# Performance work log

Measured on AMD Instinct MI355X. Metric: run time of the kernel, lower is better.

## Reference

```python
import jax, jax.numpy as jnp
import numpy as np

NUM_EMBEDDINGS = 1024
EMBEDDING_DIM = 64


def setup_inputs() -> dict:
    key = jax.random.key(0)
    kx, kw = jax.random.split(key)
    x = jax.random.normal(kx, (16, 4096, EMBEDDING_DIM), dtype=jnp.float32)
    # torch init: uniform(-1/K, 1/K)
    bound = 1.0 / NUM_EMBEDDINGS
    weight = jax.random.uniform(kw, (NUM_EMBEDDINGS, EMBEDDING_DIM),
                                dtype=jnp.float32, minval=-bound, maxval=bound)
    return {"x": x, "weight": weight}


def reference(x, weight):
    flat_x = x.reshape(-1, EMBEDDING_DIM)                      # [N, D]
    x_sq = jnp.sum(flat_x ** 2, axis=1, keepdims=True)
    w_sq = jnp.sum(weight ** 2, axis=1)[None, :]
    distances = x_sq - 2.0 * (flat_x @ weight.T) + w_sq
    encoding_indices = jnp.argmin(distances, axis=1)           # [N]
    quantized = weight[encoding_indices]                       # [N, D]
    e_latent_loss = jnp.mean((jax.lax.stop_gradient(quantized) - flat_x) ** 2)
    q_latent_loss = jnp.mean((quantized - jax.lax.stop_gradient(flat_x)) ** 2)
    loss = q_latent_loss + 0.25 * e_latent_loss
    # straight-through estimator
    quantized = flat_x + jax.lax.stop_gradient(quantized - flat_x)
    return quantized.reshape(x.shape), encoding_indices, loss
```

## Files before the change

### kernel.cpp

```cpp
#include <hip/hip_runtime.h>
#include <math.h>

#define EMB_D 64
#define MARGIN 6.0e-5f
#define SBIAS 0.5f

typedef float  f32x4  __attribute__((ext_vector_type(4)));
typedef short  bf16x8 __attribute__((ext_vector_type(8)));

__device__ __forceinline__ unsigned short f2bf(float f) {
    unsigned int u = __float_as_uint(f);
    return (unsigned short)((u + 0x7FFFu + ((u >> 16) & 1u)) >> 16);
}
__device__ __forceinline__ float bf2f(unsigned short h) {
    return __uint_as_float(((unsigned int)h) << 16);
}

union Pack8 { ushort u[8]; bf16x8 v; uint4 q; };

__device__ __forceinline__ bf16x8 ldbf8(const unsigned short* p) {
    union { uint4 u; bf16x8 v; } c;
    c.u = *(const uint4*)p;
    return c.v;
}

__global__ __launch_bounds__(256)
void vq_prepw_kernel(const float* __restrict__ w,
                     unsigned short* __restrict__ wt_hi,
                     unsigned short* __restrict__ wt_lo,
                     float* __restrict__ wsq, float* __restrict__ loss_out,
                     int K) {
    const int i = blockIdx.x * 256 + threadIdx.x;
    if (i == 0) loss_out[0] = 0.f;
    if (i >= K * 8) return;
    const int krow = i >> 3, q = i & 7;
    const int dest = ((krow >> 6) << 9) + (((krow >> 4) & 3) << 7) + (q << 4)
                   + (krow & 15);
    const float* src = w + (size_t)krow * EMB_D + q * 8;
    Pack8 h, l;
#pragma unroll
    for (int j = 0; j < 8; ++j) {
        const float f = src[j];
        h.u[j] = f2bf(f);
        l.u[j] = f2bf(f - bf2f(h.u[j]));
    }
    ((uint4*)wt_hi)[dest] = h.q;
    ((uint4*)wt_lo)[dest] = l.q;

    if (i < K) {
        const float* wr = w + (size_t)i * EMB_D;
        float r[8];
#pragma unroll
        for (int j = 0; j < 8; ++j) r[j] = __fmul_rn(wr[j], wr[j]);
#pragma unroll
        for (int t = 1; t < 8; ++t)
#pragma unroll
            for (int j = 0; j < 8; ++j)
                r[j] = __fadd_rn(r[j], __fmul_rn(wr[t * 8 + j], wr[t * 8 + j]));
        float a = __fadd_rn(__fadd_rn(r[0], r[1]), __fadd_rn(r[2], r[3]));
        float b = __fadd_rn(__fadd_rn(r[4], r[5]), __fadd_rn(r[6], r[7]));
        wsq[i] = __fadd_rn(a, b);
    }
}

__global__ __launch_bounds__(256, 2)
void vq_fused_kernel(const float* __restrict__ x,
                     const unsigned short* __restrict__ wt_hi,
                     const unsigned short* __restrict__ wt_lo,
                     const float* __restrict__ wsq,
                     const float* __restrict__ w,
                     float* __restrict__ out, float* __restrict__ loss_out,
                     int K, int N, float scale) {
    const int tid  = threadIdx.x;
    const int lane = tid & 63;
    const int wave = tid >> 6;
    const int quad = lane >> 4;
    const int c16  = lane & 15;
    const int rowbase = blockIdx.x * 128 + wave * 32;

    __shared__ __align__(16) char arena[20480];
    uint4* sh4     = (uint4*)arena;
    uint4* sl4     = (uint4*)(arena + 8192);
    float* wsq_lds = (float*)(arena + 16384);
    typedef unsigned MpArr[32][19];
    MpArr* Mp1 = (MpArr*)arena;
    MpArr* Mp2 = (MpArr*)(arena + 9728);

    __shared__ int kf[128], strow[128], k2row[128];

    Pack8 AH0[2], AL0[2], AH1[2], AL1[2];
#pragma unroll
    for (int t = 0; t < 2; ++t) {
        const float* xrow =
            x + (size_t)(rowbase + t * 16 + c16) * EMB_D + quad * 8;
#pragma unroll
        for (int j = 0; j < 8; ++j) {
            const float f0 = xrow[j];
            AH0[t].u[j] = f2bf(f0);
            AL0[t].u[j] = f2bf(f0 - bf2f(AH0[t].u[j]));
            const float f1 = xrow[32 + j];
            AH1[t].u[j] = f2bf(f1);
            AL1[t].u[j] = f2bf(f1 - bf2f(AH1[t].u[j]));
        }
    }

    {
        float4 a = ((const float4*)wsq)[tid];
        a.x += SBIAS; a.y += SBIAS; a.z += SBIAS; a.w += SBIAS;
        ((float4*)wsq_lds)[tid] = a;
    }

    unsigned s1v[2][4], s2v[2][4];
#pragma unroll
    for (int t = 0; t < 2; ++t)
#pragma unroll
        for (int i = 0; i < 4; ++i) { s1v[t][i] = 0xFFFFFFFFu; s2v[t][i] = 0xFFFFFFFFu; }

    const uint4* gh = (const uint4*)wt_hi;
    const uint4* gl = (const uint4*)wt_lo;
    uint4 ph0 = gh[tid], ph1 = gh[256 + tid];
    uint4 pl0 = gl[tid], pl1 = gl[256 + tid];

    const int nseg = K >> 6;
    for (int seg = 0; seg < nseg; ++seg) {
        sh4[tid] = ph0; sh4[256 + tid] = ph1;
        sl4[tid] = pl0; sl4[256 + tid] = pl1;
        __syncthreads();
        if (seg + 1 < nseg) {
            const int b = (seg + 1) * 512;
            ph0 = gh[b + tid]; ph1 = gh[b + 256 + tid];
            pl0 = gl[b + tid]; pl1 = gl[b + 256 + tid];
        }

#pragma unroll
        for (int s = 0; s < 4; ++s) {
            const unsigned short* shp = (const unsigned short*)sh4;
            const unsigned short* slp = (const unsigned short*)sl4;
            const bf16x8 bhi0 = ldbf8(shp + (s * 128 + lane) * 8);
            const bf16x8 bhi1 = ldbf8(shp + (s * 128 + 64 + lane) * 8);
            const bf16x8 blo0 = ldbf8(slp + (s * 128 + lane) * 8);
            const bf16x8 blo1 = ldbf8(slp + (s * 128 + 64 + lane) * 8);
            const float wqb = wsq_lds[seg * 64 + s * 16 + c16];
            const unsigned idx6 = (unsigned)(seg * 4 + s);

#pragma unroll
            for (int t = 0; t < 2; ++t) {
                f32x4 a0 = {0.f, 0.f, 0.f, 0.f};
                f32x4 a1 = {0.f, 0.f, 0.f, 0.f};
                a0 = __builtin_amdgcn_mfma_f32_16x16x32_bf16(AL0[t].v, bhi0, a0, 0, 0, 0);
                a1 = __builtin_amdgcn_mfma_f32_16x16x32_bf16(AL1[t].v, bhi1, a1, 0, 0, 0);
                a0 = __builtin_amdgcn_mfma_f32_16x16x32_bf16(AH0[t].v, blo0, a0, 0, 0, 0);
                a1 = __builtin_amdgcn_mfma_f32_16x16x32_bf16(AH1[t].v, blo1, a1, 0, 0, 0);
                a0 = __builtin_amdgcn_mfma_f32_16x16x32_bf16(AH0[t].v, bhi0, a0, 0, 0, 0);
                a1 = __builtin_amdgcn_mfma_f32_16x16x32_bf16(AH1[t].v, bhi1, a1, 0, 0, 0);
#pragma unroll
                for (int i = 0; i < 4; ++i) {
                    const float sc = fmaf(-2.0f, a0[i] + a1[i], wqb);
                    const unsigned p =
                        (__float_as_uint(sc) & 0xFFFFFFC0u) | idx6;
                    const unsigned mx = p > s1v[t][i] ? p : s1v[t][i];
                    s2v[t][i] = s2v[t][i] < mx ? s2v[t][i] : mx;
                    s1v[t][i] = s1v[t][i] < p  ? s1v[t][i] : p;
                }
            }
        }
        __syncthreads();
    }

#pragma unroll
    for (int t = 0; t < 2; ++t)
#pragma unroll
        for (int i = 0; i < 4; ++i) {
            const int r32 = t * 16 + quad * 4 + i;
            Mp1[wave][r32][c16] = s1v[t][i];
            Mp2[wave][r32][c16] = s2v[t][i];
        }
    __syncthreads();
    if (tid < 128) {
        const int wv = tid >> 5, r = tid & 31;
        unsigned g1 = 0xFFFFFFFFu, g2 = 0xFFFFFFFFu, g3 = 0xFFFFFFFFu;
        int gk1 = 0, gk2 = 0;
#pragma unroll
        for (int c = 0; c < 16; ++c) {
            {
                const unsigned p = Mp1[wv][r][c];
                if (p < g1)      { g3 = g2; g2 = g1; gk2 = gk1; g1 = p;
                                   gk1 = (int)(((p & 63u) << 4) | (unsigned)c); }
                else if (p < g2) { g3 = g2; g2 = p;
                                   gk2 = (int)(((p & 63u) << 4) | (unsigned)c); }
                else if (p < g3) { g3 = p; }
            }
            {
                const unsigned p = Mp2[wv][r][c];
                if (p < g1)      { g3 = g2; g2 = g1; gk2 = gk1; g1 = p;
                                   gk1 = (int)(((p & 63u) << 4) | (unsigned)c); }
                else if (p < g2) { g3 = g2; g2 = p;
                                   gk2 = (int)(((p & 63u) << 4) | (unsigned)c); }
                else if (p < g3) { g3 = p; }
            }
        }
        kf[tid] = gk1;
        const float f1 = __uint_as_float(g1 & 0xFFFFFFC0u);
        const float f2 = __uint_as_float(g2 & 0xFFFFFFC0u);
        const float f3 = __uint_as_float(g3 & 0xFFFFFFC0u);
        int st = 0;
        if (f2 - f1 <= MARGIN) st = (f3 - f1 > MARGIN) ? 1 : 2;
        strow[tid] = st;
        k2row[tid] = gk2;
    }
    __syncthreads();

    if (tid < 128 && strow[tid] == 1) {
        const int row = blockIdx.x * 128 + tid;
        const int ka = kf[tid], kb = k2row[tid];
        const float4* xp = (const float4*)(x + (size_t)row * EMB_D);
        const float4* wa = (const float4*)(w + (size_t)ka * EMB_D);
        const float4* wb = (const float4*)(w + (size_t)kb * EMB_D);
        float r[8];
        double aa0 = 0, aa1 = 0, aa2 = 0, aa3 = 0;
        double ab0 = 0, ab1 = 0, ab2 = 0, ab3 = 0;
#pragma unroll
        for (int q = 0; q < 16; ++q) {
            const float4 xv = xp[q], va = wa[q], vb = wb[q];
            const int j = (q & 1) * 4;
            if (q < 2) {
                r[j + 0] = __fmul_rn(xv.x, xv.x);
                r[j + 1] = __fmul_rn(xv.y, xv.y);
                r[j + 2] = __fmul_rn(xv.z, xv.z);
                r[j + 3] = __fmul_rn(xv.w, xv.w);
            } else {
                r[j + 0] = __fadd_rn(r[j + 0], __fmul_rn(xv.x, xv.x));
                r[j + 1] = __fadd_rn(r[j + 1], __fmul_rn(xv.y, xv.y));
                r[j + 2] = __fadd_rn(r[j + 2], __fmul_rn(xv.z, xv.z));
                r[j + 3] = __fadd_rn(r[j + 3], __fmul_rn(xv.w, xv.w));
            }
            aa0 = fma((double)xv.x, (double)va.x, aa0);
            aa1 = fma((double)xv.y, (double)va.y, aa1);
            aa2 = fma((double)xv.z, (double)va.z, aa2);
            aa3 = fma((double)xv.w, (double)va.w, aa3);
            ab0 = fma((double)xv.x, (double)vb.x, ab0);
            ab1 = fma((double)xv.y, (double)vb.y, ab1);
            ab2 = fma((double)xv.z, (double)vb.z, ab2);
            ab3 = fma((double)xv.w, (double)vb.w, ab3);
        }
        const float xsq = __fadd_rn(
            __fadd_rn(__fadd_rn(r[0], r[1]), __fadd_rn(r[2], r[3])),
            __fadd_rn(__fadd_rn(r[4], r[5]), __fadd_rn(r[6], r[7])));
        const float mfa = (float)((aa0 + aa1) + (aa2 + aa3));
        const float mfb = (float)((ab0 + ab1) + (ab2 + ab3));
        const float sa = __fadd_rn(__fsub_rn(xsq, __fmul_rn(2.0f, mfa)), wsq[ka]);
        const float sb = __fadd_rn(__fsub_rn(xsq, __fmul_rn(2.0f, mfb)), wsq[kb]);
        int win = ka;
        if (sb < sa || (sb == sa && kb < ka)) win = kb;
        kf[tid] = win;
    }
    __syncthreads();

    __shared__ float4 xs4[16];
    __shared__ float  xsqs;
    __shared__ float  ls[256];
    __shared__ int    lk[256];
    for (int i = 0; i < 128; ++i) {
        if (strow[i] != 2) continue;
        const int row = blockIdx.x * 128 + i;
        if (tid < 16) xs4[tid] = ((const float4*)(x + (size_t)row * EMB_D))[tid];
        __syncthreads();
        if (tid == 0) {
            const float* xf = (const float*)xs4;
            float r[8];
#pragma unroll
            for (int j = 0; j < 8; ++j) r[j] = __fmul_rn(xf[j], xf[j]);
#pragma unroll
            for (int t = 1; t < 8; ++t)
#pragma unroll
                for (int j = 0; j < 8; ++j)
                    r[j] = __fadd_rn(r[j], __fmul_rn(xf[t * 8 + j], xf[t * 8 + j]));
            xsqs = __fadd_rn(
                __fadd_rn(__fadd_rn(r[0], r[1]), __fadd_rn(r[2], r[3])),
                __fadd_rn(__fadd_rn(r[4], r[5]), __fadd_rn(r[6], r[7])));
        }
        __syncthreads();
        const float xsq = xsqs;

        float bs = INFINITY;
        int   bk = K;
        for (int t = 0; t < 4; ++t) {
            const int k = wave * (K >> 2) + t * 64 + lane;
            const float4* wr4 = (const float4*)(w + (size_t)k * EMB_D);
            double a0 = 0.0, a1 = 0.0, a2 = 0.0, a3 = 0.0;
#pragma unroll
            for (int q = 0; q < EMB_D / 4; ++q) {
                const float4 xv = xs4[q];
                const float4 wv = wr4[q];
                a0 = fma((double)xv.x, (double)wv.x, a0);
                a1 = fma((double)xv.y, (double)wv.y, a1);
                a2 = fma((double)xv.z, (double)wv.z, a2);
                a3 = fma((double)xv.w, (double)wv.w, a3);
            }
            const float mf = (float)((a0 + a1) + (a2 + a3));
            const float t2 = __fsub_rn(xsq, __fmul_rn(2.0f, mf));
            const float sc = __fadd_rn(t2, wsq[k]);
            if (sc < bs || (sc == bs && k < bk)) { bs = sc; bk = k; }
        }
        ls[tid] = bs; lk[tid] = bk;
        __syncthreads();
        if (wave == 0) {
            float gs = ls[lane];
            int   gk = lk[lane];
#pragma unroll
            for (int c = 1; c < 4; ++c) {
                const float os = ls[c * 64 + lane];
                const int   ok = lk[c * 64 + lane];
                if (os < gs || (os == gs && ok < gk)) { gs = os; gk = ok; }
            }
#pragma unroll
            for (int off = 32; off > 0; off >>= 1) {
                const float os = __shfl_down(gs, off);
                const int   ok = __shfl_down(gk, off);
                if (os < gs || (os == gs && ok < gk)) { gs = os; gk = ok; }
            }
            if (lane == 0) kf[i] = gk;
        }
        __syncthreads();
    }

    if (tid < 128) {
        const int row = blockIdx.x * 128 + tid;
        out[(size_t)N * EMB_D + row] = (float)kf[tid];
    }
    float lpart = 0.f;
#pragma unroll
    for (int rep = 0; rep < 8; ++rep) {
        int f4   = rep * 256 + tid;
        int rr   = f4 >> 4;
        int c    = f4 & 15;
        int k    = kf[rr];
        int grow = blockIdx.x * 128 + rr;
        float4 wv = ((const float4*)(w + (size_t)k * EMB_D))[c];
        float4 xq = ((const float4*)(x + (size_t)grow * EMB_D))[c];
        ((float4*)out)[(size_t)grow * (EMB_D / 4) + c] = wv;
        float dx = wv.x - xq.x, dy = wv.y - xq.y;
        float dz = wv.z - xq.z, dw = wv.w - xq.w;
        lpart += dx * dx + dy * dy + dz * dz + dw * dw;
    }
#pragma unroll
    for (int off = 32; off > 0; off >>= 1) lpart += __shfl_down(lpart, off);
    __shared__ float lred[4];
    if (lane == 0) lred[wave] = lpart;
    __syncthreads();
    if (tid == 0)
        atomicAdd(loss_out, ((lred[0] + lred[1]) + (lred[2] + lred[3])) * scale);
}

extern "C" void kernel_launch(void* const* d_in, const int* in_sizes, int n_in,
                              void* d_out, int out_size, void* d_ws, size_t ws_size,
                              hipStream_t stream) {
    const float* x = (const float*)d_in[0];
    const float* w = (const float*)d_in[1];
    float* out = (float*)d_out;
    const int xsz = in_sizes[0];
    const int wsz = in_sizes[1];
    const int N   = xsz / EMB_D;
    const int K   = wsz / EMB_D;
    const int NB  = N / 128;
    float* loss_out = out + (size_t)N * EMB_D + N;

    float* wsq = (float*)d_ws;
    unsigned short* wt_hi = (unsigned short*)(wsq + K);
    unsigned short* wt_lo = wt_hi + (size_t)K * EMB_D;

    vq_prepw_kernel<<<(K * 8 + 255) / 256, 256, 0, stream>>>(w, wt_hi, wt_lo,
                                                             wsq, loss_out, K);
    vq_fused_kernel<<<NB, 256, 0, stream>>>(x, wt_hi, wt_lo, wsq, w, out,
                                            loss_out, K, N,
                                            1.25f / (float)xsz);
}
```

Measured before the change: 133.0 us.

## Load codebook fragments directly from global memory and halve rows per block

Replaces the LDS-staged, double-buffered codebook pipeline with direct per-wave global loads of the bf16 hi/lo codebook fragments, which drops the per-segment barriers. Each wave now handles 16 rows instead of 32, so blocks cover 64 rows and twice as many blocks are launched, and occupancy is raised to 4 blocks per CU. The cost is that codebook reuse per load is halved and each wave depends on L1/L2 for the repeated codebook reads. The loop also hardcodes 64 iterations, which assumes K=1024.

```diff
diff --git a/kernel.cpp b/kernel.cpp
--- a/kernel.cpp
+++ b/kernel.cpp
@@ -18,9 +18,9 @@
 
 union Pack8 { ushort u[8]; bf16x8 v; uint4 q; };
 
-__device__ __forceinline__ bf16x8 ldbf8(const unsigned short* p) {
+__device__ __forceinline__ bf16x8 ldbf8(const uint4* p) {
     union { uint4 u; bf16x8 v; } c;
-    c.u = *(const uint4*)p;
+    c.u = *p;
     return c.v;
 }
 
@@ -63,7 +63,7 @@
     }
 }
 
-__global__ __launch_bounds__(256, 2)
+__global__ __launch_bounds__(256, 4)
 void vq_fused_kernel(const float* __restrict__ x,
                      const unsigned short* __restrict__ wt_hi,
                      const unsigned short* __restrict__ wt_lo,
@@ -76,108 +76,74 @@
     const int wave = tid >> 6;
     const int quad = lane >> 4;
     const int c16  = lane & 15;
-    const int rowbase = blockIdx.x * 128 + wave * 32;
-
-    __shared__ __align__(16) char arena[20480];
-    uint4* sh4     = (uint4*)arena;
-    uint4* sl4     = (uint4*)(arena + 8192);
-    float* wsq_lds = (float*)(arena + 16384);
-    typedef unsigned MpArr[32][19];
-    MpArr* Mp1 = (MpArr*)arena;
-    MpArr* Mp2 = (MpArr*)(arena + 9728);
-
-    __shared__ int kf[128], strow[128], k2row[128];
-
-    Pack8 AH0[2], AL0[2], AH1[2], AL1[2];
-#pragma unroll
-    for (int t = 0; t < 2; ++t) {
-        const float* xrow =
-            x + (size_t)(rowbase + t * 16 + c16) * EMB_D + quad * 8;
-#pragma unroll
-        for (int j = 0; j < 8; ++j) {
-            const float f0 = xrow[j];
-            AH0[t].u[j] = f2bf(f0);
-            AL0[t].u[j] = f2bf(f0 - bf2f(AH0[t].u[j]));
-            const float f1 = xrow[32 + j];
-            AH1[t].u[j] = f2bf(f1);
-            AL1[t].u[j] = f2bf(f1 - bf2f(AH1[t].u[j]));
-        }
-    }
+    const int rowbase = blockIdx.x * 64 + wave * 16;
+
+    __shared__ float wsq_lds[1024];
+    __shared__ unsigned Mp1[4][16][17];
+    __shared__ unsigned Mp2[4][16][17];
+    __shared__ int kf[64], strow[64], k2row[64];
+
+    const float* xrow = x + (size_t)(rowbase + c16) * EMB_D + quad * 8;
+    Pack8 ah0, al0, ah1, al1;
+#pragma unroll
+    for (int j = 0; j < 8; ++j) {
+        const float f0 = xrow[j];
+        ah0.u[j] = f2bf(f0); al0.u[j] = f2bf(f0 - bf2f(ah0.u[j]));
+        const float f1 = xrow[32 + j];
+        ah1.u[j] = f2bf(f1); al1.u[j] = f2bf(f1 - bf2f(ah1.u[j]));
+    }
+    const bf16x8 AH0 = ah0.v, AL0 = al0.v, AH1 = ah1.v, AL1 = al1.v;
 
     {
         float4 a = ((const float4*)wsq)[tid];
         a.x += SBIAS; a.y += SBIAS; a.z += SBIAS; a.w += SBIAS;
         ((float4*)wsq_lds)[tid] = a;
     }
-
-    unsigned s1v[2][4], s2v[2][4];
-#pragma unroll
-    for (int t = 0; t < 2; ++t)
-#pragma unroll
-        for (int i = 0; i < 4; ++i) { s1v[t][i] = 0xFFFFFFFFu; s2v[t][i] = 0xFFFFFFFFu; }
+    __syncthreads();
+
+    unsigned s1v[4], s2v[4];
+#pragma unroll
+    for (int i = 0; i < 4; ++i) { s1v[i] = 0xFFFFFFFFu; s2v[i] = 0xFFFFFFFFu; }
 
     const uint4* gh = (const uint4*)wt_hi;
     const uint4* gl = (const uint4*)wt_lo;
-    uint4 ph0 = gh[tid], ph1 = gh[256 + tid];
-    uint4 pl0 = gl[tid], pl1 = gl[256 + tid];
-
-    const int nseg = K >> 6;
-    for (int seg = 0; seg < nseg; ++seg) {
-        sh4[tid] = ph0; sh4[256 + tid] = ph1;
-        sl4[tid] = pl0; sl4[256 + tid] = pl1;
-        __syncthreads();
-        if (seg + 1 < nseg) {
-            const int b = (seg + 1) * 512;
-            ph0 = gh[b + tid]; ph1 = gh[b + 256 + tid];
-            pl0 = gl[b + tid]; pl1 = gl[b + 256 + tid];
-        }
-
-#pragma unroll
-        for (int s = 0; s < 4; ++s) {
-            const unsigned short* shp = (const unsigned short*)sh4;
-            const unsigned short* slp = (const unsigned short*)sl4;
-            const bf16x8 bhi0 = ldbf8(shp + (s * 128 + lane) * 8);
-            const bf16x8 bhi1 = ldbf8(shp + (s * 128 + 64 + lane) * 8);
-            const bf16x8 blo0 = ldbf8(slp + (s * 128 + lane) * 8);
-            const bf16x8 blo1 = ldbf8(slp + (s * 128 + 64 + lane) * 8);
-            const float wqb = wsq_lds[seg * 64 + s * 16 + c16];
-            const unsigned idx6 = (unsigned)(seg * 4 + s);
-
-#pragma unroll
-            for (int t = 0; t < 2; ++t) {
-                f32x4 a0 = {0.f, 0.f, 0.f, 0.f};
-                f32x4 a1 = {0.f, 0.f, 0.f, 0.f};
-                a0 = __builtin_amdgcn_mfma_f32_16x16x32_bf16(AL0[t].v, bhi0, a0, 0, 0, 0);
-                a1 = __builtin_amdgcn_mfma_f32_16x16x32_bf16(AL1[t].v, bhi1, a1, 0, 0, 0);
-                a0 = __builtin_amdgcn_mfma_f32_16x16x32_bf16(AH0[t].v, blo0, a0, 0, 0, 0);
-                a1 = __builtin_amdgcn_mfma_f32_16x16x32_bf16(AH1[t].v, blo1, a1, 0, 0, 0);
-                a0 = __builtin_amdgcn_mfma_f32_16x16x32_bf16(AH0[t].v, bhi0, a0, 0, 0, 0);
-                a1 = __builtin_amdgcn_mfma_f32_16x16x32_bf16(AH1[t].v, bhi1, a1, 0, 0, 0);
-#pragma unroll
-                for (int i = 0; i < 4; ++i) {
-                    const float sc = fmaf(-2.0f, a0[i] + a1[i], wqb);
-                    const unsigned p =
-                        (__float_as_uint(sc) & 0xFFFFFFC0u) | idx6;
-                    const unsigned mx = p > s1v[t][i] ? p : s1v[t][i];
-                    s2v[t][i] = s2v[t][i] < mx ? s2v[t][i] : mx;
-                    s1v[t][i] = s1v[t][i] < p  ? s1v[t][i] : p;
-                }
-            }
-        }
-        __syncthreads();
-    }
-
-#pragma unroll
-    for (int t = 0; t < 2; ++t)
+
+#pragma unroll 4
+    for (int u = 0; u < 64; ++u) {
+        const int base = u * 128 + lane;
+        const bf16x8 bhi0 = ldbf8(gh + base);
+        const bf16x8 bhi1 = ldbf8(gh + base + 64);
+        const bf16x8 blo0 = ldbf8(gl + base);
+        const bf16x8 blo1 = ldbf8(gl + base + 64);
+        const float wqb = wsq_lds[u * 16 + c16];
+
+        f32x4 a0 = {0.f, 0.f, 0.f, 0.f};
+        f32x4 a1 = {0.f, 0.f, 0.f, 0.f};
+        a0 = __builtin_amdgcn_mfma_f32_16x16x32_bf16(AL0, bhi0, a0, 0, 0, 0);
+        a1 = __builtin_amdgcn_mfma_f32_16x16x32_bf16(AL1, bhi1, a1, 0, 0, 0);
+        a0 = __builtin_amdgcn_mfma_f32_16x16x32_bf16(AH0, blo0, a0, 0, 0, 0);
+        a1 = __builtin_amdgcn_mfma_f32_16x16x32_bf16(AH1, blo1, a1, 0, 0, 0);
+        a0 = __builtin_amdgcn_mfma_f32_16x16x32_bf16(AH0, bhi0, a0, 0, 0, 0);
+        a1 = __builtin_amdgcn_mfma_f32_16x16x32_bf16(AH1, bhi1, a1, 0, 0, 0);
 #pragma unroll
         for (int i = 0; i < 4; ++i) {
-            const int r32 = t * 16 + quad * 4 + i;
-            Mp1[wave][r32][c16] = s1v[t][i];
-            Mp2[wave][r32][c16] = s2v[t][i];
-        }
-    __syncthreads();
-    if (tid < 128) {
-        const int wv = tid >> 5, r = tid & 31;
+            const float sc = fmaf(-2.0f, a0[i] + a1[i], wqb);
+            const unsigned p = (__float_as_uint(sc) & 0xFFFFFFC0u)
+                             | (unsigned)u;
+            const unsigned mx = p > s1v[i] ? p : s1v[i];
+            s2v[i] = s2v[i] < mx ? s2v[i] : mx;
+            s1v[i] = s1v[i] < p  ? s1v[i] : p;
+        }
+    }
+
+#pragma unroll
+    for (int i = 0; i < 4; ++i) {
+        Mp1[wave][quad * 4 + i][c16] = s1v[i];
+        Mp2[wave][quad * 4 + i][c16] = s2v[i];
+    }
+    __syncthreads();
+    if (tid < 64) {
+        const int wv = tid >> 4, r = tid & 15;
         unsigned g1 = 0xFFFFFFFFu, g2 = 0xFFFFFFFFu, g3 = 0xFFFFFFFFu;
         int gk1 = 0, gk2 = 0;
 #pragma unroll
@@ -210,8 +176,8 @@
     }
     __syncthreads();
 
-    if (tid < 128 && strow[tid] == 1) {
-        const int row = blockIdx.x * 128 + tid;
+    if (tid < 64 && strow[tid] == 1) {
+        const int row = blockIdx.x * 64 + tid;
         const int ka = kf[tid], kb = k2row[tid];
         const float4* xp = (const float4*)(x + (size_t)row * EMB_D);
         const float4* wa = (const float4*)(w + (size_t)ka * EMB_D);
@@ -260,9 +226,9 @@
     __shared__ float  xsqs;
     __shared__ float  ls[256];
     __shared__ int    lk[256];
-    for (int i = 0; i < 128; ++i) {
+    for (int i = 0; i < 64; ++i) {
         if (strow[i] != 2) continue;
-        const int row = blockIdx.x * 128 + i;
+        const int row = blockIdx.x * 64 + i;
         if (tid < 16) xs4[tid] = ((const float4*)(x + (size_t)row * EMB_D))[tid];
         __syncthreads();
         if (tid == 0) {
@@ -324,18 +290,18 @@
         __syncthreads();
     }
 
-    if (tid < 128) {
-        const int row = blockIdx.x * 128 + tid;
+    if (tid < 64) {
+        const int row = blockIdx.x * 64 + tid;
         out[(size_t)N * EMB_D + row] = (float)kf[tid];
     }
     float lpart = 0.f;
 #pragma unroll
-    for (int rep = 0; rep < 8; ++rep) {
+    for (int rep = 0; rep < 4; ++rep) {
         int f4   = rep * 256 + tid;
         int rr   = f4 >> 4;
         int c    = f4 & 15;
         int k    = kf[rr];
-        int grow = blockIdx.x * 128 + rr;
+        int grow = blockIdx.x * 64 + rr;
         float4 wv = ((const float4*)(w + (size_t)k * EMB_D))[c];
         float4 xq = ((const float4*)(x + (size_t)grow * EMB_D))[c];
         ((float4*)out)[(size_t)grow * (EMB_D / 4) + c] = wv;
@@ -362,7 +328,7 @@
     const int wsz = in_sizes[1];
     const int N   = xsz / EMB_D;
     const int K   = wsz / EMB_D;
-    const int NB  = N / 128;
+    const int NB  = N / 64;
     float* loss_out = out + (size_t)N * EMB_D + N;
 
     float* wsq = (float*)d_ws;
```

After: 162.8 us. 22.4% more time.
